# Kernel tuning notes

Hardware: AMD Instinct MI355X
Metric: run time of the kernel (lower is better)

The kernel has to match this reference:

```python
import jax, jax.numpy as jnp
import numpy as np

B, S, D, H = 4, 1024, 1024, 16
HD = D // H
LN_EPS = 1e-5


def setup_inputs() -> dict:
    key = jax.random.key(0)
    ks = jax.random.split(key, 16)
    def lin(k, fan_in, fan_out):
        bound = 1.0 / np.sqrt(fan_in)
        kw, kb = jax.random.split(k)
        W = jax.random.uniform(kw, (fan_in, fan_out), jnp.float32, -bound, bound)
        b = jax.random.uniform(kb, (fan_out,), jnp.float32, -bound, bound)
        return W, b
    W_attn, b_attn = lin(ks[0], D, 3 * D)   # self-attn fused QKV
    W_Q, b_Q = lin(ks[1], D, D)             # cross-attn Q
    W_KV, b_KV = lin(ks[2], D, 2 * D)       # cross-attn KV
    W1, b1 = lin(ks[3], D, 4 * D)           # FFN up
    W2, b2 = lin(ks[4], 4 * D, D)           # FFN down
    return {
        'en': jax.random.normal(ks[5], (B, S, D), jnp.float32),
        'fr': jax.random.normal(ks[6], (B, S, D), jnp.float32),
        'W_attn': W_attn, 'b_attn': b_attn,
        'W_Q': W_Q, 'b_Q': b_Q, 'W_KV': W_KV, 'b_KV': b_KV,
        'ln_g': jnp.ones((D,), jnp.float32), 'ln_b': jnp.zeros((D,), jnp.float32),
        'W1': W1, 'b1': b1, 'W2': W2, 'b2': b2,
        'l_en': jax.random.randint(ks[7], (B,), 1, S + 1, jnp.int32),
        'l_fr': jax.random.randint(ks[8], (B,), 1, S + 1, jnp.int32),
    }


def _masked_softmax(s):
    # softmax with rows that may be entirely -inf -> all-zero row (torch softmax + nan_to_num)
    m = jnp.max(s, axis=-1, keepdims=True)
    m = jnp.where(jnp.isfinite(m), m, 0.0)
    e = jnp.exp(s - m)  # exp(-inf) = 0
    z = jnp.sum(e, axis=-1, keepdims=True)
    return jnp.where(z > 0, e / jnp.where(z > 0, z, 1.0), 0.0)


def _layer_norm(x, g, b):
    mu = jnp.mean(x, axis=-1, keepdims=True)
    var = jnp.mean((x - mu) ** 2, axis=-1, keepdims=True)
    return (x - mu) * jax.lax.rsqrt(var + LN_EPS) * g + b


def _attend(q, k, v, mask):
    # q,k,v: [B,H,S,hd]; mask: [B,1|H broadcastable,S,S] of {0,1}
    scores = jnp.einsum('bhqd,bhkd->bhqk', q, k) / (D ** 0.5)  # NOTE: scaled by sqrt(D), as in source
    scores = jnp.where(mask == 0, -jnp.inf, scores)
    p = _masked_softmax(scores)
    out = jnp.einsum('bhqk,bhkd->bhqd', p, v)
    return out.transpose(0, 2, 1, 3).reshape(q.shape[0], q.shape[2], D)


def _valid(l):
    return (jnp.arange(S)[None, :] < l[:, None]).astype(jnp.float32)  # [B,S]


def reference(en, fr, W_attn, b_attn, W_Q, b_Q, W_KV, b_KV, ln_g, ln_b, W1, b1, W2, b2, l_en, l_fr):
    # dropout layers are identity in eval/reference mode
    v_en, v_fr = _valid(l_en), _valid(l_fr)

    # --- masked causal self-attention on fr ---
    rc = fr
    qkv = (fr @ W_attn + b_attn).reshape(B, S, 3, H, HD).transpose(2, 0, 3, 1, 4)
    q, k, v = qkv[0], qkv[1], qkv[2]
    pad = (v_fr[:, :, None] * v_fr[:, None, :])[:, None]            # [B,1,S,S]
    causal = jnp.tril(jnp.ones((S, S), jnp.float32))[None, None]    # [1,1,S,S]
    x = _attend(q, k, v, pad * causal)
    fr2 = _layer_norm(x + rc, ln_g, ln_b)

    # --- encoder-decoder cross attention ---
    rc = fr2
    q = (fr2 @ W_Q + b_Q).reshape(B, S, H, HD).transpose(0, 2, 1, 3)
    kv = (en @ W_KV + b_KV).reshape(B, S, 2, H, HD).transpose(2, 0, 3, 1, 4)
    k, v = kv[0], kv[1]
    cross = (v_fr[:, :, None] * v_en[:, None, :])[:, None]          # [B,1,S,S]
    x = _attend(q, k, v, cross)
    fr3 = _layer_norm(x + rc, ln_g, ln_b)

    # --- FFN (Linear->ReLU->Linear) then extra ReLU, residual, LN ---
    rc = fr3
    h = jax.nn.relu(fr3 @ W1 + b1) @ W2 + b2
    h = jax.nn.relu(h)
    fr4 = _layer_norm(h + rc, ln_g, ln_b)
    return fr4
```

## Files before the change

kernel.cpp:

```cpp
#include <hip/hip_runtime.h>
#include <hip/hip_bf16.h>
#include <cstdint>
#include <cstddef>

#define S_LEN  1024
#define DMODEL 1024
#define NHEAD  16
#define HDIM   64
#define BATCH  4
#define MROWS  (BATCH * S_LEN)

typedef __bf16 bf16;
typedef __attribute__((ext_vector_type(8))) __bf16 bf16x8;
typedef __attribute__((ext_vector_type(4))) __bf16 bf16x4;
typedef __attribute__((ext_vector_type(4))) float f32x4;
typedef __attribute__((ext_vector_type(4))) unsigned int u32x4;

__device__ __forceinline__ void async_load16(const void* g, void* l) {
    __builtin_amdgcn_global_load_lds(
        (const __attribute__((address_space(1))) unsigned int*)g,
        (__attribute__((address_space(3))) unsigned int*)l,
        16, 0, 0);
}

__global__ __launch_bounds__(256)
void prep_all(const float* __restrict__ fr, bf16* __restrict__ fr_bf,
              const float* __restrict__ en, bf16* __restrict__ en_bf,
              const float* __restrict__ Wa, bf16* __restrict__ Ta,
              const float* __restrict__ Wq, bf16* __restrict__ Tq,
              const float* __restrict__ Wkv, bf16* __restrict__ Tkv,
              const float* __restrict__ W1, bf16* __restrict__ T1,
              const float* __restrict__ W2, bf16* __restrict__ T2) {
    __shared__ float t[32][33];
    int id = blockIdx.x;
    if (id < 8192) {
        const int n4 = MROWS * DMODEL / 4;
        int i = id * 256 + threadIdx.x;
        const float* in = fr; bf16* out = fr_bf;
        if (i >= n4) { i -= n4; in = en; out = en_bf; }
        f32x4 v = ((const f32x4*)in)[i];
        bf16x4 o;
#pragma unroll
        for (int e = 0; e < 4; ++e) o[e] = (bf16)v[e];
        ((bf16x4*)out)[i] = o;
        return;
    }
    id -= 8192;
    const float* W; bf16* Wt; int K, N, nx, base;
    if (id < 3072)       { W = Wa;  Wt = Ta;  K = 1024; N = 3072; nx = 96;  base = 0; }
    else if (id < 4096)  { W = Wq;  Wt = Tq;  K = 1024; N = 1024; nx = 32;  base = 3072; }
    else if (id < 6144)  { W = Wkv; Wt = Tkv; K = 1024; N = 2048; nx = 64;  base = 4096; }
    else if (id < 10240) { W = W1;  Wt = T1;  K = 1024; N = 4096; nx = 128; base = 6144; }
    else                 { W = W2;  Wt = T2;  K = 4096; N = 1024; nx = 32;  base = 10240; }
    int loc = id - base;
    int n0 = (loc % nx) * 32, k0 = (loc / nx) * 32;
    int tx = threadIdx.x & 31, ty = threadIdx.x >> 5;
#pragma unroll
    for (int j = 0; j < 4; ++j)
        t[ty + j * 8][tx] = W[(size_t)(k0 + ty + j * 8) * N + n0 + tx];
    __syncthreads();
#pragma unroll
    for (int j = 0; j < 4; ++j)
        Wt[(size_t)(n0 + ty + j * 8) * K + k0 + tx] = (bf16)t[tx][ty + j * 8];
}

__device__ __forceinline__ void gemm_acc(const bf16* __restrict__ A,
                                         const bf16* __restrict__ Bt,
                                         int Klen, int lda, int ldb,
                                         bf16* Alds, bf16* Blds,
                                         f32x4 acc[4][4]) {
    const int tid = threadIdx.x;
    const int wave = tid >> 6, lane = tid & 63;
    const int wr = wave >> 1, wc = wave & 1;
    const int lr = lane & 15, lg = lane >> 4, lk = lg * 8;
    const int srow = lane >> 2, scol = (lane & 3) * 8;

    const bf16* Aw = A + (size_t)(wave * 32 + srow) * lda + scol;
    const bf16* Bw = Bt + (size_t)(wave * 32 + srow) * ldb + scol;
    const int ldsw = (wave * 32) * 32;

    async_load16(Aw, Alds + ldsw);
    async_load16(Aw + (size_t)16 * lda, Alds + ldsw + 16 * 32);
    async_load16(Bw, Blds + ldsw);
    async_load16(Bw + (size_t)16 * ldb, Blds + ldsw + 16 * 32);
    __syncthreads();

    const int nt = Klen >> 5;
    for (int t = 0; t < nt; ++t) {
        const int cur = t & 1;
        if (t + 1 < nt) {
            const size_t k0 = (size_t)(t + 1) << 5;
            bf16* Ad = Alds + (cur ^ 1) * (128 * 32) + ldsw;
            bf16* Bd = Blds + (cur ^ 1) * (128 * 32) + ldsw;
            async_load16(Aw + k0, Ad);
            async_load16(Aw + (size_t)16 * lda + k0, Ad + 16 * 32);
            async_load16(Bw + k0, Bd);
            async_load16(Bw + (size_t)16 * ldb + k0, Bd + 16 * 32);
        }
        const bf16* Ab = Alds + cur * (128 * 32);
        const bf16* Bb = Blds + cur * (128 * 32);
        bf16x8 af[4], bfv[4];
#pragma unroll
        for (int i = 0; i < 4; ++i) {
            af[i]  = *(const bf16x8*)&Ab[(wr * 64 + i * 16 + lr) * 32 + lk];
            bfv[i] = *(const bf16x8*)&Bb[(wc * 64 + i * 16 + lr) * 32 + lk];
        }
#pragma unroll
        for (int mi = 0; mi < 4; ++mi)
#pragma unroll
            for (int ni = 0; ni < 4; ++ni)
                acc[mi][ni] = __builtin_amdgcn_mfma_f32_16x16x32_bf16(
                    af[mi], bfv[ni], acc[mi][ni], 0, 0, 0);
        __syncthreads();
    }
}

template<bool RELU>
__device__ __forceinline__ void epi_bf16(bf16* __restrict__ C, const float* __restrict__ bias,
                                         int N, int m0, int n0, f32x4 acc[4][4]) {
    const int tid = threadIdx.x;
    const int wave = tid >> 6, lane = tid & 63;
    const int wr = wave >> 1, wc = wave & 1;
    const int lr = lane & 15, lg = lane >> 4;
#pragma unroll
    for (int ni = 0; ni < 4; ++ni) {
        int n = n0 + wc * 64 + ni * 16 + lr;
        float bn = bias[n];
#pragma unroll
        for (int mi = 0; mi < 4; ++mi)
#pragma unroll
            for (int r = 0; r < 4; ++r) {
                int m = m0 + wr * 64 + mi * 16 + lg * 4 + r;
                float v = acc[mi][ni][r] + bn;
                if (RELU) v = v > 0.f ? v : 0.f;
                C[(size_t)m * N + n] = (bf16)v;
            }
    }
}

__device__ __forceinline__ bool tile_dead(const int* Lm, int m0) {
    if (!Lm) return false;
    int cap = (Lm[m0 >> 10] + 63) & ~63;
    return (m0 & 1023) >= cap;
}

template<bool RELU>
__global__ __launch_bounds__(256, 2)
void gemm_one(const bf16* __restrict__ A, const bf16* __restrict__ Bt,
              const float* __restrict__ bias, bf16* __restrict__ C,
              int N, int K, const int* __restrict__ Lm) {
    __shared__ alignas(16) bf16 Alds[2][128 * 32];
    __shared__ alignas(16) bf16 Blds[2][128 * 32];
    const int nwg = gridDim.x;
    const int flat = blockIdx.x;
    const int swz = (flat & 7) * (nwg >> 3) + (flat >> 3);
    const int m0 = (swz & 31) * 128, n0 = (swz >> 5) * 128;
    if (tile_dead(Lm, m0)) return;
    f32x4 acc[4][4] = {};
    gemm_acc(A + (size_t)m0 * K, Bt + (size_t)n0 * K, K, K, K,
             &Alds[0][0], &Blds[0][0], acc);
    epi_bf16<RELU>(C, bias, N, m0, n0, acc);
}

struct GemmArgs {
    const bf16* A; const bf16* Bt; const float* bias; bf16* C;
    int N; int K; const int* Lm;
};
__global__ __launch_bounds__(256, 2)
void gemm_dual(GemmArgs g0, int nwg0, GemmArgs g1) {
    __shared__ alignas(16) bf16 Alds[2][128 * 32];
    __shared__ alignas(16) bf16 Blds[2][128 * 32];
    const int nwg = gridDim.x;
    const int flat = blockIdx.x;
    const int swz = (flat & 7) * (nwg >> 3) + (flat >> 3);
    const bool first = swz < nwg0;
    const GemmArgs g = first ? g0 : g1;
    const int f = first ? swz : swz - nwg0;
    const int m0 = (f & 31) * 128, n0 = (f >> 5) * 128;
    if (tile_dead(g.Lm, m0)) return;
    f32x4 acc[4][4] = {};
    gemm_acc(g.A + (size_t)m0 * g.K, g.Bt + (size_t)n0 * g.K, g.K, g.K, g.K,
             &Alds[0][0], &Blds[0][0], acc);
    epi_bf16<false>(g.C, g.bias, g.N, m0, n0, acc);
}

__global__ __launch_bounds__(256, 2)
void gemm_splitk2(const bf16* __restrict__ A, const bf16* __restrict__ Bt,
                  float* __restrict__ P0, float* __restrict__ P1,
                  int N, int K, int nwg_half) {
    __shared__ alignas(16) bf16 Alds[2][128 * 32];
    __shared__ alignas(16) bf16 Blds[2][128 * 32];
    const int nwg = gridDim.x;
    const int flat = blockIdx.x;
    const int swz = (flat & 7) * (nwg >> 3) + (flat >> 3);
    const int kz = swz >= nwg_half ? 1 : 0;
    const int f = swz - kz * nwg_half;
    const int m0 = (f & 31) * 128, n0 = (f >> 5) * 128;
    const int Kh = K >> 1;
    const size_t koff = (size_t)kz * Kh;
    f32x4 acc[4][4] = {};
    gemm_acc(A + (size_t)m0 * K + koff, Bt + (size_t)n0 * K + koff, Kh, K, K,
             &Alds[0][0], &Blds[0][0], acc);
    float* P = kz ? P1 : P0;
    const int tid = threadIdx.x;
    const int wave = tid >> 6, lane = tid & 63;
    const int wr = wave >> 1, wc = wave & 1;
    const int lr = lane & 15, lg = lane >> 4;
#pragma unroll
    for (int ni = 0; ni < 4; ++ni) {
        int n = n0 + wc * 64 + ni * 16 + lr;
#pragma unroll
        for (int mi = 0; mi < 4; ++mi)
#pragma unroll
            for (int r = 0; r < 4; ++r) {
                int m = m0 + wr * 64 + mi * 16 + lg * 4 + r;
                P[(size_t)m * N + n] = acc[mi][ni][r];
            }
    }
}

template<bool CAUSAL>
__global__ __launch_bounds__(256, 4)
void attn_flash(const bf16* __restrict__ Qp, int qs,
                const bf16* __restrict__ Kp, int ks,
                const bf16* __restrict__ Vp, int vs,
                const int* __restrict__ Lq, const int* __restrict__ Lk,
                bf16* __restrict__ Op) {
    __shared__ alignas(16) bf16 Klds[64 * 64];
    __shared__ alignas(16) bf16 Vt[64 * 64];
    __shared__ alignas(16) bf16 Plds[4][16 * 64];

    const int tid = threadIdx.x;
    const int wave = tid >> 6, lane = tid & 63;
    const int qt = blockIdx.x, h = blockIdx.y, b = blockIdx.z;
    const int q0 = qt * 64;
    const int lq = Lq[b], lk = Lk[b];
    const int lr = lane & 15, lg = lane >> 4;

    if (q0 >= lq) {
#pragma unroll
        for (int dt = 0; dt < 4; ++dt)
#pragma unroll
            for (int r = 0; r < 4; ++r) {
                int q = q0 + wave * 16 + lg * 4 + r;
                Op[(size_t)(b * S_LEN + q) * DMODEL + h * HDIM + dt * 16 + lr] = (bf16)0.f;
            }
        return;
    }

    char* KldsB = (char*)Klds;
    char* VtB = (char*)Vt;
    char* PldsB = (char*)&Plds[wave][0];

    bf16x8 aq[2];
    {
        const bf16* qrow = Qp + (size_t)(b * S_LEN + q0 + wave * 16 + lr) * qs + h * HDIM;
        aq[0] = *(const bf16x8*)(qrow + 0 + lg * 8);
        aq[1] = *(const bf16x8*)(qrow + 32 + lg * 8);
    }

    f32x4 o[4] = {};
    float m_run[4], l_run[4];
#pragma unroll
    for (int r = 0; r < 4; ++r) { m_run[r] = -INFINITY; l_run[r] = 0.f; }

    int kv_end = CAUSAL ? (q0 + 64) : S_LEN;
    int lk_cap = (lk + 63) & ~63;
    if (kv_end > lk_cap) kv_end = lk_cap;

    const int vk = lane;
    const int vd0 = wave * 16;

    for (int kk0 = 0; kk0 < kv_end; kk0 += 64) {
#pragma unroll
        for (int c = 0; c < 2; ++c) {
            int rloc = c * 8 + (lane >> 3);
            int row = wave * 16 + rloc;
            int chunk = (lane & 7) ^ (rloc & 7);
            async_load16(Kp + (size_t)(b * S_LEN + kk0 + row) * ks + h * HDIM + chunk * 8,
                         KldsB + (size_t)(wave * 16 + c * 8) * 128);
        }
        {
            const bf16* vsrc = Vp + (size_t)(b * S_LEN + kk0 + vk) * vs + h * HDIM + vd0;
            bf16x8 v0 = *(const bf16x8*)vsrc;
            bf16x8 v1 = *(const bf16x8*)(vsrc + 8);
#pragma unroll
            for (int e = 0; e < 8; ++e) {
                int d0 = vd0 + e, d1 = vd0 + 8 + e;
                *(bf16*)(VtB + (((size_t)d0 * 128 + vk * 2) ^ ((d0 & 7) << 4))) = v0[e];
                *(bf16*)(VtB + (((size_t)d1 * 128 + vk * 2) ^ ((d1 & 7) << 4))) = v1[e];
            }
        }
        __syncthreads();

        f32x4 sa[4];
#pragma unroll
        for (int kt = 0; kt < 4; ++kt) {
            int row = kt * 16 + lr;
            f32x4 z = {};
#pragma unroll
            for (int ds_ = 0; ds_ < 2; ++ds_) {
                bf16x8 bk = *(const bf16x8*)(KldsB +
                    (((size_t)row * 128 + ds_ * 64 + lg * 16) ^ ((row & 7) << 4)));
                z = __builtin_amdgcn_mfma_f32_16x16x32_bf16(aq[ds_], bk, z, 0, 0, 0);
            }
            sa[kt] = z;
        }

        float p[4][4];
#pragma unroll
        for (int r = 0; r < 4; ++r) {
            int q = q0 + wave * 16 + lg * 4 + r;
            float best = -INFINITY;
#pragma unroll
            for (int kt = 0; kt < 4; ++kt) {
                int kk = kk0 + kt * 16 + lr;
                float s = sa[kt][r] * 0.03125f;
                bool ok = (q < lq) && (kk < lk) && (!CAUSAL || kk <= q);
                s = ok ? s : -INFINITY;
                p[kt][r] = s;
                best = fmaxf(best, s);
            }
#pragma unroll
            for (int msk = 1; msk < 16; msk <<= 1)
                best = fmaxf(best, __shfl_xor(best, msk));
            float mn = fmaxf(m_run[r], best);
            float alpha = (m_run[r] == -INFINITY) ? 0.0f : __expf(m_run[r] - mn);
            float rs = 0.f;
#pragma unroll
            for (int kt = 0; kt < 4; ++kt) {
                float s = p[kt][r];
                float e = (s == -INFINITY) ? 0.f : __expf(s - mn);
                p[kt][r] = e;
                rs += e;
            }
#pragma unroll
            for (int msk = 1; msk < 16; msk <<= 1)
                rs += __shfl_xor(rs, msk);
            l_run[r] = l_run[r] * alpha + rs;
            m_run[r] = mn;
#pragma unroll
            for (int dt = 0; dt < 4; ++dt) o[dt][r] *= alpha;
        }

#pragma unroll
        for (int kt = 0; kt < 4; ++kt)
#pragma unroll
            for (int r = 0; r < 4; ++r) {
                int ql = lg * 4 + r, kkl = kt * 16 + lr;
                *(bf16*)(PldsB + (((size_t)ql * 128 + kkl * 2) ^ ((ql & 7) << 4))) =
                    (bf16)p[kt][r];
            }
        bf16x8 pa[2];
#pragma unroll
        for (int ksl = 0; ksl < 2; ++ksl)
            pa[ksl] = *(const bf16x8*)(PldsB +
                (((size_t)lr * 128 + ksl * 64 + lg * 16) ^ ((lr & 7) << 4)));

#pragma unroll
        for (int dt = 0; dt < 4; ++dt) {
            int row = dt * 16 + lr;
#pragma unroll
            for (int ksl = 0; ksl < 2; ++ksl) {
                bf16x8 bv = *(const bf16x8*)(VtB +
                    (((size_t)row * 128 + ksl * 64 + lg * 16) ^ ((row & 7) << 4)));
                o[dt] = __builtin_amdgcn_mfma_f32_16x16x32_bf16(pa[ksl], bv, o[dt], 0, 0, 0);
            }
        }
        __syncthreads();
    }

#pragma unroll
    for (int dt = 0; dt < 4; ++dt) {
#pragma unroll
        for (int r = 0; r < 4; ++r) {
            int q = q0 + wave * 16 + lg * 4 + r;
            float denom = l_run[r];
            float val = denom > 0.f ? o[dt][r] / denom : 0.f;
            Op[(size_t)(b * S_LEN + q) * DMODEL + h * HDIM + dt * 16 + lr] = (bf16)val;
        }
    }
}

__global__ __launch_bounds__(256)
void ln_kernel(const bf16* __restrict__ x, const float* __restrict__ rc,
               const float* __restrict__ g, const float* __restrict__ beta,
               float* __restrict__ yf, bf16* __restrict__ yb) {
    const int row = blockIdx.x;
    const int tid = threadIdx.x;
    const int wave = tid >> 6, lane = tid & 63;
    const bf16* xr = x + (size_t)row * DMODEL;
    const float* rr = rc + (size_t)row * DMODEL;

    float v[4];
    {
        bf16x4 xv = *(const bf16x4*)(xr + tid * 4);
        f32x4 rv = *(const f32x4*)(rr + tid * 4);
#pragma unroll
        for (int i = 0; i < 4; ++i) v[i] = (float)xv[i] + rv[i];
    }
    float s = v[0] + v[1] + v[2] + v[3];
    float s2 = v[0] * v[0] + v[1] * v[1] + v[2] * v[2] + v[3] * v[3];
#pragma unroll
    for (int msk = 1; msk < 64; msk <<= 1) {
        s += __shfl_xor(s, msk);
        s2 += __shfl_xor(s2, msk);
    }
    __shared__ float red[8];
    if (lane == 0) { red[wave] = s; red[4 + wave] = s2; }
    __syncthreads();
    float ts = red[0] + red[1] + red[2] + red[3];
    float ts2 = red[4] + red[5] + red[6] + red[7];
    float mean = ts * (1.f / DMODEL);
    float var = ts2 * (1.f / DMODEL) - mean * mean;
    float inv = rsqrtf(var + 1e-5f);
#pragma unroll
    for (int i = 0; i < 4; ++i) {
        int c = tid * 4 + i;
        float yv = (v[i] - mean) * inv * g[c] + beta[c];
        if (yf) yf[(size_t)row * DMODEL + c] = yv;
        if (yb) yb[(size_t)row * DMODEL + c] = (bf16)yv;
    }
}

__global__ __launch_bounds__(256)
void ln_splitk(const float* __restrict__ P0, const float* __restrict__ P1,
               const float* __restrict__ bias, const float* __restrict__ rc,
               const float* __restrict__ g, const float* __restrict__ beta,
               float* __restrict__ yf) {
    const int row = blockIdx.x;
    const int tid = threadIdx.x;
    const int wave = tid >> 6, lane = tid & 63;
    const size_t off = (size_t)row * DMODEL + tid * 4;

    f32x4 a = *(const f32x4*)(P0 + off);
    f32x4 bb = *(const f32x4*)(P1 + off);
    f32x4 bi = *(const f32x4*)(bias + tid * 4);
    f32x4 rv = *(const f32x4*)(rc + off);
    float v[4];
#pragma unroll
    for (int i = 0; i < 4; ++i) {
        float h = a[i] + bb[i] + bi[i];
        h = h > 0.f ? h : 0.f;
        v[i] = h + rv[i];
    }
    float s = v[0] + v[1] + v[2] + v[3];
    float s2 = v[0] * v[0] + v[1] * v[1] + v[2] * v[2] + v[3] * v[3];
#pragma unroll
    for (int msk = 1; msk < 64; msk <<= 1) {
        s += __shfl_xor(s, msk);
        s2 += __shfl_xor(s2, msk);
    }
    __shared__ float red[8];
    if (lane == 0) { red[wave] = s; red[4 + wave] = s2; }
    __syncthreads();
    float ts = red[0] + red[1] + red[2] + red[3];
    float ts2 = red[4] + red[5] + red[6] + red[7];
    float mean = ts * (1.f / DMODEL);
    float var = ts2 * (1.f / DMODEL) - mean * mean;
    float inv = rsqrtf(var + 1e-5f);
#pragma unroll
    for (int i = 0; i < 4; ++i) {
        int c = tid * 4 + i;
        yf[(size_t)row * DMODEL + c] = (v[i] - mean) * inv * g[c] + beta[c];
    }
}

extern "C" void kernel_launch(void* const* d_in, const int* in_sizes, int n_in,
                              void* d_out, int out_size, void* d_ws, size_t ws_size,
                              hipStream_t stream) {
    const float* en     = (const float*)d_in[0];
    const float* fr     = (const float*)d_in[1];
    const float* W_attn = (const float*)d_in[2];
    const float* b_attn = (const float*)d_in[3];
    const float* W_Q    = (const float*)d_in[4];
    const float* b_Q    = (const float*)d_in[5];
    const float* W_KV   = (const float*)d_in[6];
    const float* b_KV   = (const float*)d_in[7];
    const float* ln_g   = (const float*)d_in[8];
    const float* ln_b   = (const float*)d_in[9];
    const float* W1     = (const float*)d_in[10];
    const float* b1     = (const float*)d_in[11];
    const float* W2     = (const float*)d_in[12];
    const float* b2     = (const float*)d_in[13];
    const int* l_en     = (const int*)d_in[14];
    const int* l_fr     = (const int*)d_in[15];
    float* out = (float*)d_out;

    char* ws = (char*)d_ws;
    const size_t MB = (size_t)1 << 20;
    bf16* Wt_attn = (bf16*)(ws + 0);
    bf16* Wt_Q    = (bf16*)(ws + 6 * MB);
    bf16* Wt_KV   = (bf16*)(ws + 8 * MB);
    bf16* Wt_1    = (bf16*)(ws + 12 * MB);
    bf16* Wt_2    = (bf16*)(ws + 20 * MB);
    bf16* fr_bf   = (bf16*)(ws + 28 * MB);
    bf16* en_bf   = (bf16*)(ws + 36 * MB);
    bf16* bigA    = (bf16*)(ws + 44 * MB);
    bf16* xbuf    = (bf16*)(ws + 76 * MB);
    float* fr2    = (float*)(ws + 84 * MB);
    float* fr3    = (float*)(ws + 100 * MB);
    bf16* fbx     = (bf16*)(ws + 116 * MB);
    float* P0 = (float*)(ws + 0);
    float* P1 = (float*)(ws + 28 * MB);
    bf16* kvc = (bf16*)(ws + 100 * MB);

    dim3 blk(256);

    prep_all<<<dim3(22528), blk, 0, stream>>>(fr, fr_bf, en, en_bf,
        W_attn, Wt_attn, W_Q, Wt_Q, W_KV, Wt_KV, W1, Wt_1, W2, Wt_2);

    bf16* qkv = bigA;
    GemmArgs gq{fr_bf, Wt_attn, b_attn, qkv, 3072, 1024, l_fr};
    GemmArgs gk{en_bf, Wt_KV, b_KV, kvc, 2048, 1024, l_en};
    gemm_dual<<<dim3(1280), blk, 0, stream>>>(gq, 768, gk);

    attn_flash<true><<<dim3(16, NHEAD, BATCH), blk, 0, stream>>>(
        qkv, 3072, qkv + 1024, 3072, qkv + 2048, 3072, l_fr, l_fr, xbuf);
    ln_kernel<<<dim3(4096), blk, 0, stream>>>(xbuf, fr, ln_g, ln_b, fr2, fbx);

    bf16* qc = bigA;
    gemm_one<false><<<dim3(256), blk, 0, stream>>>(fbx, Wt_Q, b_Q, qc, 1024, 1024, l_fr);
    attn_flash<false><<<dim3(16, NHEAD, BATCH), blk, 0, stream>>>(
        qc, 1024, kvc, 2048, kvc + 1024, 2048, l_fr, l_en, xbuf);
    ln_kernel<<<dim3(4096), blk, 0, stream>>>(xbuf, fr2, ln_g, ln_b, fr3, fbx);

    bf16* h = bigA;
    gemm_one<true><<<dim3(1024), blk, 0, stream>>>(fbx, Wt_1, b1, h, 4096, 1024, nullptr);
    gemm_splitk2<<<dim3(512), blk, 0, stream>>>(h, Wt_2, P0, P1, 1024, 4096, 256);
    ln_splitk<<<dim3(4096), blk, 0, stream>>>(P0, P1, b2, fr3, ln_g, ln_b, out);
}
```

Measured before the change: 302.0 us.

## Overlap late weight transposes with first GEMM and use BK=64 swizzled LDS tiles

The transposes of W_Q, W1 and W2 move out of the prep kernel and into extra trailing blocks of the first dual GEMM launch. That work can then fill idle CUs alongside the QKV/KV GEMM instead of sitting on the critical path before it. A new K=64 GEMM main loop with XOR-swizzled LDS layout is added and used for the Q projection and split-K FFN down GEMM. It aims to halve barrier count per K and avoid LDS bank conflicts, at the cost of doubling LDS per block, which may lower occupancy.

```diff
diff --git a/kernel.cpp b/kernel.cpp
--- a/kernel.cpp
+++ b/kernel.cpp
@@ -27,10 +27,7 @@
 void prep_all(const float* __restrict__ fr, bf16* __restrict__ fr_bf,
               const float* __restrict__ en, bf16* __restrict__ en_bf,
               const float* __restrict__ Wa, bf16* __restrict__ Ta,
-              const float* __restrict__ Wq, bf16* __restrict__ Tq,
-              const float* __restrict__ Wkv, bf16* __restrict__ Tkv,
-              const float* __restrict__ W1, bf16* __restrict__ T1,
-              const float* __restrict__ W2, bf16* __restrict__ T2) {
+              const float* __restrict__ Wkv, bf16* __restrict__ Tkv) {
     __shared__ float t[32][33];
     int id = blockIdx.x;
     if (id < 8192) {
@@ -47,11 +44,8 @@
     }
     id -= 8192;
     const float* W; bf16* Wt; int K, N, nx, base;
-    if (id < 3072)       { W = Wa;  Wt = Ta;  K = 1024; N = 3072; nx = 96;  base = 0; }
-    else if (id < 4096)  { W = Wq;  Wt = Tq;  K = 1024; N = 1024; nx = 32;  base = 3072; }
-    else if (id < 6144)  { W = Wkv; Wt = Tkv; K = 1024; N = 2048; nx = 64;  base = 4096; }
-    else if (id < 10240) { W = W1;  Wt = T1;  K = 1024; N = 4096; nx = 128; base = 6144; }
-    else                 { W = W2;  Wt = T2;  K = 4096; N = 1024; nx = 32;  base = 10240; }
+    if (id < 3072) { W = Wa;  Wt = Ta;  K = 1024; N = 3072; nx = 96; base = 0; }
+    else           { W = Wkv; Wt = Tkv; K = 1024; N = 2048; nx = 64; base = 3072; }
     int loc = id - base;
     int n0 = (loc % nx) * 32, k0 = (loc / nx) * 32;
     int tx = threadIdx.x & 31, ty = threadIdx.x >> 5;
@@ -113,6 +107,65 @@
                     af[mi], bfv[ni], acc[mi][ni], 0, 0, 0);
         __syncthreads();
     }
+}
+
+__device__ __forceinline__ void gemm_acc64(const bf16* __restrict__ A,
+                                           const bf16* __restrict__ Bt,
+                                           int Klen, int lda, int ldb,
+                                           bf16* Alds, bf16* Blds,
+                                           f32x4 acc[4][4]) {
+    const int tid = threadIdx.x;
+    const int wave = tid >> 6, lane = tid & 63;
+    const int wr = wave >> 1, wc = wave & 1;
+    const int lr = lane & 15, lg = lane >> 4;
+    const int srow = lane >> 3;
+    const int sch = (lane & 7) ^ srow;
+
+    const bf16* Aw = A + (size_t)(wave * 32 + srow) * lda + sch * 8;
+    const bf16* Bw = Bt + (size_t)(wave * 32 + srow) * ldb + sch * 8;
+
+    const int nt = Klen >> 6;
+#define STAGE64(buf, k0)                                                       \
+    {                                                                          \
+        bf16* Ad = Alds + (buf) * (128 * 64) + (wave * 32) * 64;               \
+        bf16* Bd = Blds + (buf) * (128 * 64) + (wave * 32) * 64;               \
+        _Pragma("unroll")                                                      \
+        for (int j = 0; j < 4; ++j) {                                          \
+            async_load16(Aw + (size_t)(j * 8) * lda + (k0), Ad + (j * 8) * 64);\
+            async_load16(Bw + (size_t)(j * 8) * ldb + (k0), Bd + (j * 8) * 64);\
+        }                                                                      \
+    }
+
+    STAGE64(0, 0);
+    __syncthreads();
+
+    for (int t = 0; t < nt; ++t) {
+        const int cur = t & 1;
+        if (t + 1 < nt) STAGE64(cur ^ 1, (size_t)(t + 1) << 6);
+        const char* Ab = (const char*)(Alds + cur * (128 * 64));
+        const char* Bb = (const char*)(Blds + cur * (128 * 64));
+#pragma unroll
+        for (int ks = 0; ks < 2; ++ks) {
+            bf16x8 af[4], bfv[4];
+#pragma unroll
+            for (int i = 0; i < 4; ++i) {
+                int ra = wr * 64 + i * 16 + lr;
+                int rb = wc * 64 + i * 16 + lr;
+                af[i] = *(const bf16x8*)(Ab + (size_t)ra * 128 +
+                          ((ks * 64 + lg * 16) ^ ((ra & 7) << 4)));
+                bfv[i] = *(const bf16x8*)(Bb + (size_t)rb * 128 +
+                          ((ks * 64 + lg * 16) ^ ((rb & 7) << 4)));
+            }
+#pragma unroll
+            for (int mi = 0; mi < 4; ++mi)
+#pragma unroll
+                for (int ni = 0; ni < 4; ++ni)
+                    acc[mi][ni] = __builtin_amdgcn_mfma_f32_16x16x32_bf16(
+                        af[mi], bfv[ni], acc[mi][ni], 0, 0, 0);
+        }
+        __syncthreads();
+    }
+#undef STAGE64
 }
 
 template<bool RELU>
@@ -162,17 +215,56 @@
     epi_bf16<RELU>(C, bias, N, m0, n0, acc);
 }
 
+template<bool RELU>
+__global__ __launch_bounds__(256, 2)
+void gemm_one64(const bf16* __restrict__ A, const bf16* __restrict__ Bt,
+                const float* __restrict__ bias, bf16* __restrict__ C,
+                int N, int K, const int* __restrict__ Lm) {
+    __shared__ alignas(16) bf16 Alds[2][128 * 64];
+    __shared__ alignas(16) bf16 Blds[2][128 * 64];
+    const int nwg = gridDim.x;
+    const int flat = blockIdx.x;
+    const int swz = (flat & 7) * (nwg >> 3) + (flat >> 3);
+    const int m0 = (swz & 31) * 128, n0 = (swz >> 5) * 128;
+    if (tile_dead(Lm, m0)) return;
+    f32x4 acc[4][4] = {};
+    gemm_acc64(A + (size_t)m0 * K, Bt + (size_t)n0 * K, K, K, K,
+               &Alds[0][0], &Blds[0][0], acc);
+    epi_bf16<RELU>(C, bias, N, m0, n0, acc);
+}
+
 struct GemmArgs {
     const bf16* A; const bf16* Bt; const float* bias; bf16* C;
     int N; int K; const int* Lm;
 };
 __global__ __launch_bounds__(256, 2)
-void gemm_dual(GemmArgs g0, int nwg0, GemmArgs g1) {
+void gemm_dual(GemmArgs g0, int nwg0, GemmArgs g1, int nwgG,
+               const float* __restrict__ Wq, bf16* __restrict__ Tq,
+               const float* __restrict__ W1, bf16* __restrict__ T1,
+               const float* __restrict__ W2, bf16* __restrict__ T2) {
     __shared__ alignas(16) bf16 Alds[2][128 * 32];
     __shared__ alignas(16) bf16 Blds[2][128 * 32];
-    const int nwg = gridDim.x;
     const int flat = blockIdx.x;
-    const int swz = (flat & 7) * (nwg >> 3) + (flat >> 3);
+    if (flat >= nwgG) {
+        int id = flat - nwgG;
+        const float* W; bf16* Wt; int K, N, nx, base;
+        if (id < 1024)      { W = Wq; Wt = Tq; K = 1024; N = 1024; nx = 32;  base = 0; }
+        else if (id < 5120) { W = W1; Wt = T1; K = 1024; N = 4096; nx = 128; base = 1024; }
+        else                { W = W2; Wt = T2; K = 4096; N = 1024; nx = 32;  base = 5120; }
+        int loc = id - base;
+        int n0 = (loc % nx) * 32, k0 = (loc / nx) * 32;
+        float (*t)[33] = (float(*)[33])&Alds[0][0];
+        int tx = threadIdx.x & 31, ty = threadIdx.x >> 5;
+#pragma unroll
+        for (int j = 0; j < 4; ++j)
+            t[ty + j * 8][tx] = W[(size_t)(k0 + ty + j * 8) * N + n0 + tx];
+        __syncthreads();
+#pragma unroll
+        for (int j = 0; j < 4; ++j)
+            Wt[(size_t)(n0 + ty + j * 8) * K + k0 + tx] = (bf16)t[tx][ty + j * 8];
+        return;
+    }
+    const int swz = (flat & 7) * (nwgG >> 3) + (flat >> 3);
     const bool first = swz < nwg0;
     const GemmArgs g = first ? g0 : g1;
     const int f = first ? swz : swz - nwg0;
@@ -188,8 +280,8 @@
 void gemm_splitk2(const bf16* __restrict__ A, const bf16* __restrict__ Bt,
                   float* __restrict__ P0, float* __restrict__ P1,
                   int N, int K, int nwg_half) {
-    __shared__ alignas(16) bf16 Alds[2][128 * 32];
-    __shared__ alignas(16) bf16 Blds[2][128 * 32];
+    __shared__ alignas(16) bf16 Alds[2][128 * 64];
+    __shared__ alignas(16) bf16 Blds[2][128 * 64];
     const int nwg = gridDim.x;
     const int flat = blockIdx.x;
     const int swz = (flat & 7) * (nwg >> 3) + (flat >> 3);
@@ -199,8 +291,8 @@
     const int Kh = K >> 1;
     const size_t koff = (size_t)kz * Kh;
     f32x4 acc[4][4] = {};
-    gemm_acc(A + (size_t)m0 * K + koff, Bt + (size_t)n0 * K + koff, Kh, K, K,
-             &Alds[0][0], &Blds[0][0], acc);
+    gemm_acc64(A + (size_t)m0 * K + koff, Bt + (size_t)n0 * K + koff, Kh, K, K,
+               &Alds[0][0], &Blds[0][0], acc);
     float* P = kz ? P1 : P0;
     const int tid = threadIdx.x;
     const int wave = tid >> 6, lane = tid & 63;
@@ -507,20 +599,21 @@
 
     dim3 blk(256);
 
-    prep_all<<<dim3(22528), blk, 0, stream>>>(fr, fr_bf, en, en_bf,
-        W_attn, Wt_attn, W_Q, Wt_Q, W_KV, Wt_KV, W1, Wt_1, W2, Wt_2);
+    prep_all<<<dim3(13312), blk, 0, stream>>>(fr, fr_bf, en, en_bf,
+                                              W_attn, Wt_attn, W_KV, Wt_KV);
 
     bf16* qkv = bigA;
     GemmArgs gq{fr_bf, Wt_attn, b_attn, qkv, 3072, 1024, l_fr};
     GemmArgs gk{en_bf, Wt_KV, b_KV, kvc, 2048, 1024, l_en};
-    gemm_dual<<<dim3(1280), blk, 0, stream>>>(gq, 768, gk);
+    gemm_dual<<<dim3(1280 + 9216), blk, 0, stream>>>(gq, 768, gk, 1280,
+                                                     W_Q, Wt_Q, W1, Wt_1, W2, Wt_2);
 
     attn_flash<true><<<dim3(16, NHEAD, BATCH), blk, 0, stream>>>(
         qkv, 3072, qkv + 1024, 3072, qkv + 2048, 3072, l_fr, l_fr, xbuf);
     ln_kernel<<<dim3(4096), blk, 0, stream>>>(xbuf, fr, ln_g, ln_b, fr2, fbx);
 
     bf16* qc = bigA;
-    gemm_one<false><<<dim3(256), blk, 0, stream>>>(fbx, Wt_Q, b_Q, qc, 1024, 1024, l_fr);
+    gemm_one64<false><<<dim3(256), blk, 0, stream>>>(fbx, Wt_Q, b_Q, qc, 1024, 1024, l_fr);
     attn_flash<false><<<dim3(16, NHEAD, BATCH), blk, 0, stream>>>(
         qc, 1024, kvc, 2048, kvc + 1024, 2048, l_fr, l_en, xbuf);
     ln_kernel<<<dim3(4096), blk, 0, stream>>>(xbuf, fr2, ln_g, ln_b, fr3, fbx);
```

Measured after the change: 285.7 us. -5.4%, faster.
